# Optimization experiments

Hardware: AMD Instinct MI355X
Metric: run time of the kernel (lower is better)

## Reference

```python
import jax, jax.numpy as jnp
import numpy as np

C = 128        # dim_in = dim_out = dim_mid (exp_ratio=1.0)
HEADS = 4      # C // dim_head
DH = 32        # dim_head
WS = 7         # window_size
EPS = 1e-6
SCALE = DH ** -0.5


def bn3d(x, g, b):
    # BatchNorm3d forward (training-mode batch stats), eps=1e-6
    m = jnp.mean(x, axis=(0, 2, 3, 4), keepdims=True)
    v = jnp.mean((x - m) ** 2, axis=(0, 2, 3, 4), keepdims=True)
    xn = (x - m) * jax.lax.rsqrt(v + EPS)
    return xn * g.reshape(1, -1, 1, 1, 1) + b.reshape(1, -1, 1, 1, 1)


def conv1x1(x, w):
    # 1x1x1 conv, no bias: w is (out, in)
    return jnp.einsum('oi,bihwd->bohwd', w, x)


def setup_inputs() -> dict:
    key = jax.random.key(0)
    ks = jax.random.split(key, 6)
    x = jax.random.normal(ks[0], (4, C, 28, 28, 28), jnp.float32)
    g_in = jnp.ones((C,), jnp.float32)
    b_in = jnp.zeros((C,), jnp.float32)
    w_qk = jax.random.normal(ks[1], (2 * C, C), jnp.float32) * (C ** -0.5)
    w_v = jax.random.normal(ks[2], (C, C), jnp.float32) * (C ** -0.5)
    w_cl = jax.random.normal(ks[3], (C, C, 3, 3, 3), jnp.float32) * ((C * 27) ** -0.5)
    g_cl = jnp.ones((C,), jnp.float32)
    b_cl = jnp.zeros((C,), jnp.float32)
    w_proj = jax.random.normal(ks[4], (C, C), jnp.float32) * (C ** -0.5)
    return {"x": x, "g_in": g_in, "b_in": b_in, "w_qk": w_qk, "w_v": w_v,
            "w_cl": w_cl, "g_cl": g_cl, "b_cl": b_cl, "w_proj": w_proj}


def reference(x, g_in, b_in, w_qk, w_v, w_cl, g_cl, b_cl, w_proj):
    B, Cc, H, W, D = x.shape
    shortcut = x
    x = bn3d(x, g_in, b_in)

    # strided window partition: einops '(h1 n1)' => h1 (window) is the OUTER factor
    n1, n2, n3 = H // WS, W // WS, D // WS  # chosen divisible -> zero pad
    xw = x.reshape(B, Cc, WS, n1, WS, n2, WS, n3)
    xw = xw.transpose(0, 3, 5, 7, 1, 2, 4, 6).reshape(B * n1 * n2 * n3, Cc, WS, WS, WS)
    b = xw.shape[0]
    L = WS ** 3

    # qk: 1x1 conv -> split q,k -> (b, heads, L, dh)
    qk = conv1x1(xw, w_qk).reshape(b, 2, HEADS, DH, L)
    q = qk[:, 0].transpose(0, 1, 3, 2)       # b h L d
    k = qk[:, 1]                             # b h d L
    attn = jax.nn.softmax(jnp.einsum('bhld,bhdm->bhlm', q, k) * SCALE, axis=-1)

    # v: 1x1 conv + relu (attn_pre=False)
    v = jax.nn.relu(conv1x1(xw, w_v)).reshape(b, HEADS, DH, L)  # b h d L
    xs = jnp.einsum('bhlm,bhdm->bhld', attn, v)                 # b h L d
    xs = xs.transpose(0, 1, 3, 2).reshape(b, Cc, WS, WS, WS)

    # reverse window partition
    x = xs.reshape(B, n1, n2, n3, Cc, WS, WS, WS)
    x = x.transpose(0, 4, 5, 1, 6, 2, 7, 3).reshape(B, Cc, H, W, D)

    # local 3x3x3 conv + BN + SiLU, residual (has_skip inside iRMB branch)
    y = jax.lax.conv_general_dilated(
        x, w_cl, window_strides=(1, 1, 1),
        padding=[(1, 1), (1, 1), (1, 1)],
        dimension_numbers=('NCDHW', 'OIDHW', 'NCDHW'))
    y = jax.nn.silu(bn3d(y, g_cl, b_cl))
    x = x + y  # SE is Identity (se_ratio=0)

    x = conv1x1(x, w_proj)
    return shortcut + x
```

## Files before the change

### kernel.cpp

```cpp
#include <hip/hip_runtime.h>
#include <hip/hip_bf16.h>

#define C      128
#define SP     21952
#define PT     87808
#define LW     343
#define EPS_   1e-6f
#define SCALE_ 0.17677669529663687f

#define MISC_A   0
#define MISC_B   128
#define MISC_BQK 256
#define MISC_BV  512
#define MISC_SUM 640
#define MISC_SQ  768
#define MISC_A2  896
#define MISC_B2  1024
#define MISC_XS  1152
#define MISC_XQ  1280

typedef __attribute__((ext_vector_type(8))) short bf16x8;
typedef __attribute__((ext_vector_type(4))) float f32x4;

__device__ __forceinline__ float b2f(unsigned short u){
  return __uint_as_float(((unsigned int)u) << 16);
}
__device__ __forceinline__ unsigned short f2b(float f){
  unsigned int u = __float_as_uint(f);
  u += 0x7fffu + ((u >> 16) & 1u);
  return (unsigned short)(u >> 16);
}

__global__ __launch_bounds__(256) void k0_partial(const float* __restrict__ x,
                                                  float* __restrict__ misc){
  int c = blockIdx.x & 127, chunk = blockIdx.x >> 7;
  int bb = chunk >> 1, half = chunk & 1;
  const float4* p = reinterpret_cast<const float4*>(
      x + (size_t)(bb*C + c)*SP + half*10976);
  int t = threadIdx.x;
  float s = 0.f, ss = 0.f;
  for (int i = t; i < 2744; i += 256){
    float4 v = p[i];
    s  += v.x + v.y + v.z + v.w;
    ss += v.x*v.x + v.y*v.y + v.z*v.z + v.w*v.w;
  }
  #pragma unroll
  for (int off = 32; off > 0; off >>= 1){
    s  += __shfl_xor(s,  off);
    ss += __shfl_xor(ss, off);
  }
  __shared__ float red[8];
  int wid = t >> 6, lane = t & 63;
  if (lane == 0){ red[wid] = s; red[4+wid] = ss; }
  __syncthreads();
  if (t == 0){
    atomicAdd(&misc[MISC_XS + c], red[0]+red[1]+red[2]+red[3]);
    atomicAdd(&misc[MISC_XQ + c], red[4]+red[5]+red[6]+red[7]);
  }
}

__global__ void k1_bias(const float* __restrict__ wqk, const float* __restrict__ wvv,
                        const float* __restrict__ gin, const float* __restrict__ bin,
                        float* __restrict__ misc){
  __shared__ float bv[128];
  int t = threadIdx.x;
  {
    float mean = misc[MISC_XS + t] / (float)PT;
    float var  = misc[MISC_XQ + t] / (float)PT - mean*mean;
    float a = rsqrtf(var + EPS_) * gin[t];
    float bb = bin[t] - mean * a;
    bv[t] = bb;
    if (blockIdx.x == 0){ misc[MISC_A + t] = a; misc[MISC_B + t] = bb; }
  }
  __syncthreads();
  int o = blockIdx.x*128 + t;
  float acc = 0.f;
  if (o < 256){
    const float* wr = wqk + (size_t)o*128;
    for (int c = 0; c < 128; ++c) acc += wr[c]*bv[c];
    misc[MISC_BQK + o] = acc;
  } else {
    const float* wr = wvv + (size_t)(o-256)*128;
    for (int c = 0; c < 128; ++c) acc += wr[c]*bv[c];
    misc[MISC_BV + (o-256)] = acc;
  }
}

__global__ void k1w(const float* __restrict__ wqk, const float* __restrict__ wvv,
                    unsigned short* __restrict__ w2){
  int idx = blockIdx.x*256 + threadIdx.x;
  int o = idx >> 7;
  float w = (o < 256) ? wqk[idx] : wvv[idx - 32768];
  unsigned short h = f2b(w);
  w2[idx] = h;
  w2[49152 + idx] = f2b(w - b2f(h));
}

__global__ __launch_bounds__(256) void k2_qkv(const float* __restrict__ x,
        const unsigned short* __restrict__ w2, const float* __restrict__ misc,
        unsigned short* __restrict__ qg, unsigned short* __restrict__ kg,
        unsigned short* __restrict__ vg){
  __shared__ __align__(16) unsigned short xh[8192];
  __shared__ __align__(16) unsigned short xl[8192];
  __shared__ float ascale[128];
  __shared__ unsigned int posTab[64];
  int t = threadIdx.x;
  int P0 = blockIdx.x * 64;
  int b = P0 / SP, sp0 = P0 % SP;
  if (t < 128) ascale[t] = misc[MISC_A + t];
  if (t < 64){
    int sp = sp0 + t;
    int h_ = sp / 784, rem = sp % 784;
    int w_ = rem / 28, d_ = rem % 28;
    int w1 = h_ & 3, s1 = h_ >> 2;
    int w2i = w_ & 3, s2 = w_ >> 2;
    int w3 = d_ & 3, s3 = d_ >> 2;
    int bw = ((b*4 + w1)*4 + w2i)*4 + w3;
    int l  = (s1*7 + s2)*7 + s3;
    posTab[t] = (unsigned int)(bw*43904 + l*32);
  }
  __syncthreads();
  {
    int p = t & 63;
    int ob = t >> 6;
    const float* xb = x + (size_t)b*C*SP + sp0 + p;
    for (int it = 0; it < 4; ++it){
      int c0 = (ob + it*4) * 8;
      unsigned int ph[4], pl[4];
      #pragma unroll
      for (int j = 0; j < 4; ++j){
        float f0 = xb[(size_t)(c0 + 2*j)*SP]     * ascale[c0 + 2*j];
        float f1 = xb[(size_t)(c0 + 2*j + 1)*SP] * ascale[c0 + 2*j + 1];
        unsigned short h0 = f2b(f0), h1 = f2b(f1);
        unsigned short l0 = f2b(f0 - b2f(h0)), l1 = f2b(f1 - b2f(h1));
        ph[j] = (unsigned int)h0 | ((unsigned int)h1 << 16);
        pl[j] = (unsigned int)l0 | ((unsigned int)l1 << 16);
      }
      int byte = (p*256 + c0*2) ^ ((p & 7) << 4);
      *reinterpret_cast<uint4*>((char*)xh + byte) = make_uint4(ph[0],ph[1],ph[2],ph[3]);
      *reinterpret_cast<uint4*>((char*)xl + byte) = make_uint4(pl[0],pl[1],pl[2],pl[3]);
    }
  }
  __syncthreads();
  int wid = t >> 6, lane = t & 63;
  int g = lane >> 4, ln = lane & 15;
  int wstart = wid * 96;
  f32x4 acc[6][4];
  #pragma unroll
  for (int nt = 0; nt < 6; ++nt){
    float bv = misc[256 + wstart + nt*16 + ln];
    #pragma unroll
    for (int mt = 0; mt < 4; ++mt) acc[nt][mt] = (f32x4){bv,bv,bv,bv};
  }
  #pragma unroll 1
  for (int kk = 0; kk < 4; ++kk){
    bf16x8 ah[4], al[4];
    #pragma unroll
    for (int mt = 0; mt < 4; ++mt){
      int row = mt*16 + ln;
      int byte = (row*256 + kk*64 + g*16) ^ ((ln & 7) << 4);
      ah[mt] = *reinterpret_cast<const bf16x8*>((const char*)xh + byte);
      al[mt] = *reinterpret_cast<const bf16x8*>((const char*)xl + byte);
    }
    #pragma unroll
    for (int nt = 0; nt < 6; ++nt){
      int o = wstart + nt*16 + ln;
      const unsigned short* wp = w2 + (size_t)o*128 + kk*32 + g*8;
      bf16x8 whf = *reinterpret_cast<const bf16x8*>(wp);
      bf16x8 wlf = *reinterpret_cast<const bf16x8*>(wp + 49152);
      #pragma unroll
      for (int mt = 0; mt < 4; ++mt){
        acc[nt][mt] = __builtin_amdgcn_mfma_f32_16x16x32_bf16(ah[mt], whf, acc[nt][mt], 0, 0, 0);
        acc[nt][mt] = __builtin_amdgcn_mfma_f32_16x16x32_bf16(al[mt], whf, acc[nt][mt], 0, 0, 0);
        acc[nt][mt] = __builtin_amdgcn_mfma_f32_16x16x32_bf16(ah[mt], wlf, acc[nt][mt], 0, 0, 0);
      }
    }
  }
  unsigned int ptab[16];
  #pragma unroll
  for (int mt = 0; mt < 4; ++mt)
    #pragma unroll
    for (int r = 0; r < 4; ++r)
      ptab[mt*4+r] = posTab[mt*16 + g*4 + r];
  #pragma unroll
  for (int nt = 0; nt < 6; ++nt){
    int o = wstart + nt*16 + ln;
    bool isv = (o >= 256);
    int oo = o & 127;
    unsigned short* dst = ((o < 128) ? qg : (o < 256 ? kg : vg)) + (oo >> 5)*10976 + (oo & 31);
    #pragma unroll
    for (int mt = 0; mt < 4; ++mt){
      #pragma unroll
      for (int r = 0; r < 4; ++r){
        float v = acc[nt][mt][r];
        if (isv) v = fmaxf(v, 0.f);
        dst[ptab[mt*4+r]] = f2b(v);
      }
    }
  }
}

__global__ __launch_bounds__(256) void k3_attn(const unsigned short* __restrict__ qg,
        const unsigned short* __restrict__ kg, const unsigned short* __restrict__ vg,
        unsigned short* __restrict__ xatt){
  __shared__ __align__(16) unsigned short klds[352*32];
  __shared__ __align__(16) unsigned short vper[32*360];
  __shared__ __align__(16) unsigned short pbuf[4][640];
  int bh = blockIdx.x;
  int bw = bh >> 2, h = bh & 3;
  int t = threadIdx.x;
  int wid = t >> 6, lane = t & 63;
  int g = lane >> 4, ln = lane & 15;
  const unsigned short* kbase = kg + (size_t)bh*LW*32;
  const unsigned short* vbase = vg + (size_t)bh*LW*32;
  const unsigned short* qbase = qg + (size_t)bh*LW*32;
  {
    const uint4* src = reinterpret_cast<const uint4*>(kbase);
    uint4* dst = reinterpret_cast<uint4*>(klds);
    for (int i = t; i < 1372; i += 256) dst[i] = src[i];
    for (int i = t; i < 288; i += 256) klds[10976 + i] = 0;
  }
  for (int idx = t; idx < 10976; idx += 256){
    int m = idx >> 5, d = idx & 31;
    int km = m & 31;
    int pk = ((km & 15) << 1) | (km >> 4);
    vper[d*360 + ((m >> 5) << 5) + pk] = vbase[idx];
  }
  for (int i = t; i < 288; i += 256){
    int m = 343 + (i >> 5), d = i & 31;
    int km = m & 31;
    int pk = ((km & 15) << 1) | (km >> 4);
    vper[d*360 + 320 + pk] = 0;
  }
  __syncthreads();
  int w1 = (bw>>4)&3, w2 = (bw>>2)&3, w3 = bw&3, b = bw>>6;
  unsigned short* pb = pbuf[wid];
  const f32x4 zero4 = {0.f, 0.f, 0.f, 0.f};
  for (int rt = wid; rt < 22; rt += 4){
    int row0 = rt << 4;
    bf16x8 qf = *reinterpret_cast<const bf16x8*>(qbase + (size_t)(row0 + ln)*32 + g*8);
    f32x4 s[22];
    #pragma unroll
    for (int nt = 0; nt < 22; ++nt){
      bf16x8 kf = *reinterpret_cast<const bf16x8*>(&klds[(nt*16 + ln)*32 + g*8]);
      s[nt] = __builtin_amdgcn_mfma_f32_16x16x32_bf16(qf, kf, zero4, 0, 0, 0);
    }
    float mxs[4];
    #pragma unroll
    for (int q = 0; q < 4; ++q){
      float m0 = -1e30f;
      #pragma unroll
      for (int nt = 0; nt < 21; ++nt) m0 = fmaxf(m0, s[nt][q]);
      if (ln < 7) m0 = fmaxf(m0, s[21][q]);
      #pragma unroll
      for (int off = 8; off > 0; off >>= 1) m0 = fmaxf(m0, __shfl_xor(m0, off));
      mxs[q] = m0 * SCALE_;
    }
    f32x4 o0 = zero4, o1 = zero4;
    float sums[4] = {0.f, 0.f, 0.f, 0.f};
    #pragma unroll
    for (int c = 0; c < 11; ++c){
      #pragma unroll
      for (int q = 0; q < 4; ++q){
        float e0 = __expf(fmaf(s[2*c][q],   SCALE_, -mxs[q]));
        float e1 = (c*32 + 16 + ln < 343)
                 ? __expf(fmaf(s[2*c+1][q], SCALE_, -mxs[q])) : 0.f;
        sums[q] += e0 + e1;
        unsigned int pkd;
        asm volatile("v_cvt_pk_bf16_f32 %0, %1, %2" : "=v"(pkd) : "v"(e0), "v"(e1));
        *reinterpret_cast<unsigned int*>(&pb[(g*4+q)*40 + (ln<<1)]) = pkd;
      }
      asm volatile("s_waitcnt lgkmcnt(0)" ::: "memory");
      __builtin_amdgcn_sched_barrier(0);
      bf16x8 pa  = *reinterpret_cast<const bf16x8*>(&pb[ln*40 + g*8]);
      bf16x8 vb0 = *reinterpret_cast<const bf16x8*>(&vper[ln*360       + (c<<5) + g*8]);
      bf16x8 vb1 = *reinterpret_cast<const bf16x8*>(&vper[(16+ln)*360  + (c<<5) + g*8]);
      o0 = __builtin_amdgcn_mfma_f32_16x16x32_bf16(pa, vb0, o0, 0, 0, 0);
      o1 = __builtin_amdgcn_mfma_f32_16x16x32_bf16(pa, vb1, o1, 0, 0, 0);
    }
    float iss[4];
    #pragma unroll
    for (int q = 0; q < 4; ++q){
      float sq = sums[q];
      #pragma unroll
      for (int off = 8; off > 0; off >>= 1) sq += __shfl_xor(sq, off);
      iss[q] = 1.f / sq;
    }
    #pragma unroll
    for (int q = 0; q < 4; ++q){
      int l = row0 + g*4 + q;
      if (l < 343){
        int ss1 = l/49, ss2 = (l/7)%7, ss3 = l%7;
        int sp = (ss1*4+w1)*784 + (ss2*4+w2)*28 + (ss3*4+w3);
        size_t gaddr = ((size_t)b*SP + sp)*128 + h*32;
        xatt[gaddr + ln]      = f2b(o0[q]*iss[q]);
        xatt[gaddr + 16 + ln] = f2b(o1[q]*iss[q]);
      }
    }
  }
}

__global__ void k_wprep(const float* __restrict__ wcl, unsigned short* __restrict__ wbf){
  int f = blockIdx.x*256 + threadIdx.x;
  int j  = f & 7;
  int oc = (f >> 3) & 127;
  int kgr= (f >> 10) & 7;
  int sl = f >> 13;
  int h  = sl / 27, tap = sl % 27;
  int ic = h*64 + kgr*8 + j;
  wbf[f] = f2b(wcl[((size_t)oc*128 + ic)*27 + tap]);
}

__global__ void k6w(const float* __restrict__ wproj, unsigned short* __restrict__ w6){
  int idx = blockIdx.x*256 + threadIdx.x;
  float w = wproj[idx];
  unsigned short h = f2b(w);
  w6[idx] = h;
  w6[16384 + idx] = f2b(w - b2f(h));
}

__global__ __launch_bounds__(128) void k4_mfma(const unsigned short* __restrict__ xag,
        const unsigned short* __restrict__ wbf, unsigned short* __restrict__ yg){
  __shared__ __align__(16) unsigned short halo[8*216*8];
  int t = threadIdx.x, wid = t >> 6, lane = t & 63;
  int g = lane >> 4, ln = lane & 15;
  int stile = blockIdx.x;
  int b = stile / 343, srem = stile % 343;
  int z0 = (srem/49)*4, y0 = ((srem/7)%7)*4, x0 = (srem%7)*4;
  int ohalf = wid;
  int hp = (ln>>2)*6 + (ln&3);
  f32x4 acc[4][4] = {};
  const unsigned short* wb0 = wbf + (size_t)(g*1024 + ohalf*512 + ln*8);
  bf16x8 b0[8], b1[8];

  #define BLOADX(dst_, s_) do { \
    const unsigned short* wp_ = wb0 + (size_t)(s_)*8192; \
    _Pragma("unroll") \
    for (int ks_ = 0; ks_ < 2; ++ks_) \
      _Pragma("unroll") \
      for (int nt_ = 0; nt_ < 4; ++nt_) \
        dst_[ks_*4+nt_] = *reinterpret_cast<const bf16x8*>(wp_ + ks_*4096 + nt_*128); \
  } while(0)

  #define COMPUTE(tap_, buf_) do { \
    int dz_ = (tap_)/9, r9_ = (tap_)%9, dy_ = r9_/3, dx_ = r9_%3; \
    int off_ = dz_*36 + dy_*6 + dx_; \
    bf16x8 af_[2][4]; \
    _Pragma("unroll") \
    for (int ks_ = 0; ks_ < 2; ++ks_) \
      _Pragma("unroll") \
      for (int mt_ = 0; mt_ < 4; ++mt_) \
        af_[ks_][mt_] = *reinterpret_cast<const bf16x8*>( \
            &halo[((ks_*4 + g)*216 + mt_*36 + hp + off_)*8]); \
    _Pragma("unroll") \
    for (int nt_ = 0; nt_ < 4; ++nt_) \
      _Pragma("unroll") \
      for (int ks_ = 0; ks_ < 2; ++ks_) \
        _Pragma("unroll") \
        for (int mt_ = 0; mt_ < 4; ++mt_) \
          acc[nt_][mt_] = __builtin_amdgcn_mfma_f32_16x16x32_bf16( \
              af_[ks_][mt_], buf_[ks_*4+nt_], acc[nt_][mt_], 0, 0, 0); \
  } while(0)

  int s = 0;
  BLOADX(b0, 0);
  for (int h = 0; h < 2; ++h){
    if (h) __syncthreads();
    for (int cidx = t; cidx < 1728; cidx += 128){
      int kgr = cidx / 216, pos = cidx % 216;
      int uz = pos / 36, r36 = pos % 36, uy = r36 / 6, ux = r36 % 6;
      int zz = z0 - 1 + uz, yy = y0 - 1 + uy, xx = x0 - 1 + ux;
      uint4 v = make_uint4(0u,0u,0u,0u);
      if (zz >= 0 && zz < 28 && yy >= 0 && yy < 28 && xx >= 0 && xx < 28)
        v = *reinterpret_cast<const uint4*>(
              &xag[(((size_t)b*SP) + zz*784 + yy*28 + xx)*128 + h*64 + kgr*8]);
      *reinterpret_cast<uint4*>(&halo[(size_t)cidx*8]) = v;
    }
    __syncthreads();
    for (int tp = 0; tp < 26; tp += 2){
      BLOADX(b1, s+1);
      COMPUTE(tp, b0);
      BLOADX(b0, s+2);
      COMPUTE(tp+1, b1);
      s += 2;
    }
    COMPUTE(26, b0);
    ++s;
    if (s < 54) BLOADX(b0, s);
  }
  #pragma unroll
  for (int nt = 0; nt < 4; ++nt){
    int oc = ohalf*64 + nt*16 + ln;
    #pragma unroll
    for (int mt = 0; mt < 4; ++mt){
      #pragma unroll
      for (int r = 0; r < 4; ++r){
        int pos = (z0 + mt)*784 + (y0 + g)*28 + (x0 + r);
        yg[((size_t)b*SP + pos)*128 + oc] = f2b(acc[nt][mt][r]);
      }
    }
  }
  #undef BLOADX
  #undef COMPUTE
}

__global__ __launch_bounds__(256) void k5_ystats(const unsigned short* __restrict__ yg,
                                                 float* __restrict__ misc){
  int t = threadIdx.x;
  int c8 = t & 15;
  int pr = t >> 4;
  float s[8] = {0,0,0,0,0,0,0,0}, q[8] = {0,0,0,0,0,0,0,0};
  size_t base = (size_t)blockIdx.x * 256;
  for (int i = 0; i < 16; ++i){
    size_t pos = base + i*16 + pr;
    uint4 v = *reinterpret_cast<const uint4*>(yg + pos*128 + c8*8);
    #pragma unroll
    for (int j = 0; j < 4; ++j){
      unsigned int u = (&v.x)[j];
      float f0 = __uint_as_float(u << 16);
      float f1 = __uint_as_float(u & 0xffff0000u);
      s[2*j]   += f0; q[2*j]   += f0*f0;
      s[2*j+1] += f1; q[2*j+1] += f1*f1;
    }
  }
  #pragma unroll
  for (int j = 0; j < 8; ++j){
    s[j] += __shfl_xor(s[j], 16); q[j] += __shfl_xor(q[j], 16);
    s[j] += __shfl_xor(s[j], 32); q[j] += __shfl_xor(q[j], 32);
  }
  __shared__ float rs[128], rq[128];
  if (t < 128){ rs[t] = 0.f; rq[t] = 0.f; }
  __syncthreads();
  if ((t & 48) == 0){
    #pragma unroll
    for (int j = 0; j < 8; ++j){
      atomicAdd(&rs[c8*8+j], s[j]);
      atomicAdd(&rq[c8*8+j], q[j]);
    }
  }
  __syncthreads();
  if (t < 128){
    atomicAdd(&misc[MISC_SUM + t], rs[t]);
    atomicAdd(&misc[MISC_SQ  + t], rq[t]);
  }
}

__global__ void k5b_finstats(const float* __restrict__ gcl, const float* __restrict__ bcl,
                             float* __restrict__ misc){
  int c = threadIdx.x;
  float mean = misc[MISC_SUM+c] / (float)PT;
  float var  = misc[MISC_SQ +c] / (float)PT - mean*mean;
  float a = gcl[c] * rsqrtf(var + EPS_);
  misc[MISC_A2+c] = a;
  misc[MISC_B2+c] = bcl[c] - mean*a;
}

__global__ __launch_bounds__(256) void k6_final(const unsigned short* __restrict__ xag,
        const unsigned short* __restrict__ yg, const unsigned short* __restrict__ w6,
        const float* __restrict__ xin, const float* __restrict__ misc,
        float* __restrict__ out){
  __shared__ __align__(16) unsigned short xh[8192];
  __shared__ __align__(16) unsigned short xl[8192];
  __shared__ float a2s[128], b2s[128];
  int t = threadIdx.x;
  int P0 = blockIdx.x * 64;
  int b = P0 / SP, sp0 = P0 % SP;
  if (t < 128){ a2s[t] = misc[MISC_A2+t]; b2s[t] = misc[MISC_B2+t]; }
  __syncthreads();
  for (int idx = t; idx < 1024; idx += 256){
    int p = idx >> 4, c0 = (idx & 15) * 8;
    size_t gb = (size_t)(P0 + p)*128 + c0;
    uint4 yv4 = *reinterpret_cast<const uint4*>(yg + gb);
    uint4 xa4 = *reinterpret_cast<const uint4*>(xag + gb);
    unsigned int ph[4], pl[4];
    #pragma unroll
    for (int j = 0; j < 4; ++j){
      unsigned int uy = (&yv4.x)[j], ux = (&xa4.x)[j];
      int c = c0 + 2*j;
      float y0 = __uint_as_float(uy << 16)          * a2s[c]   + b2s[c];
      float y1 = __uint_as_float(uy & 0xffff0000u)  * a2s[c+1] + b2s[c+1];
      float v0 = __uint_as_float(ux << 16)         + y0 / (1.f + __expf(-y0));
      float v1 = __uint_as_float(ux & 0xffff0000u) + y1 / (1.f + __expf(-y1));
      unsigned short h0 = f2b(v0), h1 = f2b(v1);
      unsigned short l0 = f2b(v0 - b2f(h0)), l1 = f2b(v1 - b2f(h1));
      ph[j] = (unsigned int)h0 | ((unsigned int)h1 << 16);
      pl[j] = (unsigned int)l0 | ((unsigned int)l1 << 16);
    }
    int byte = (p*256 + c0*2) ^ ((p & 7) << 4);
    *reinterpret_cast<uint4*>((char*)xh + byte) = make_uint4(ph[0],ph[1],ph[2],ph[3]);
    *reinterpret_cast<uint4*>((char*)xl + byte) = make_uint4(pl[0],pl[1],pl[2],pl[3]);
  }
  __syncthreads();
  int wid = t >> 6, lane = t & 63;
  int g = lane >> 4, ln = lane & 15;
  f32x4 acc[2][4] = {};
  #pragma unroll 1
  for (int kk = 0; kk < 4; ++kk){
    bf16x8 bh[4], bl[4];
    #pragma unroll
    for (int pt = 0; pt < 4; ++pt){
      int row = pt*16 + ln;
      int byte = (row*256 + kk*64 + g*16) ^ ((ln & 7) << 4);
      bh[pt] = *reinterpret_cast<const bf16x8*>((const char*)xh + byte);
      bl[pt] = *reinterpret_cast<const bf16x8*>((const char*)xl + byte);
    }
    #pragma unroll
    for (int ot = 0; ot < 2; ++ot){
      int o = wid*32 + ot*16 + ln;
      const unsigned short* wp = w6 + (size_t)o*128 + kk*32 + g*8;
      bf16x8 wh = *reinterpret_cast<const bf16x8*>(wp);
      bf16x8 wl = *reinterpret_cast<const bf16x8*>(wp + 16384);
      #pragma unroll
      for (int pt = 0; pt < 4; ++pt){
        acc[ot][pt] = __builtin_amdgcn_mfma_f32_16x16x32_bf16(wh, bh[pt], acc[ot][pt], 0, 0, 0);
        acc[ot][pt] = __builtin_amdgcn_mfma_f32_16x16x32_bf16(wl, bh[pt], acc[ot][pt], 0, 0, 0);
        acc[ot][pt] = __builtin_amdgcn_mfma_f32_16x16x32_bf16(wh, bl[pt], acc[ot][pt], 0, 0, 0);
      }
    }
  }
  #pragma unroll
  for (int ot = 0; ot < 2; ++ot){
    #pragma unroll
    for (int r = 0; r < 4; ++r){
      int o = wid*32 + ot*16 + g*4 + r;
      size_t gbase = ((size_t)b*128 + o)*SP + sp0;
      #pragma unroll
      for (int pt = 0; pt < 4; ++pt){
        size_t gaddr = gbase + pt*16 + ln;
        out[gaddr] = xin[gaddr] + acc[ot][pt][r];
      }
    }
  }
}

extern "C" void kernel_launch(void* const* d_in, const int* in_sizes, int n_in,
                              void* d_out, int out_size, void* d_ws, size_t ws_size,
                              hipStream_t stream){
  const float* x      = (const float*)d_in[0];
  const float* g_in   = (const float*)d_in[1];
  const float* b_in   = (const float*)d_in[2];
  const float* w_qk   = (const float*)d_in[3];
  const float* w_v    = (const float*)d_in[4];
  const float* w_cl   = (const float*)d_in[5];
  const float* g_cl   = (const float*)d_in[6];
  const float* b_cl   = (const float*)d_in[7];
  const float* w_proj = (const float*)d_in[8];
  float* out = (float*)d_out;

  char* ws = (char*)d_ws;
  unsigned short* qg  = (unsigned short*)ws;
  unsigned short* kgp = qg  + 11239424;
  unsigned short* vg  = kgp + 11239424;
  unsigned short* xag = vg  + 11239424;
  unsigned short* yg  = xag + 11239424;
  float* misc = (float*)(ws + (size_t)5*22478848);
  unsigned short* wbf = qg;
  unsigned short* w6  = qg + 524288;
  unsigned short* w2  = yg;

  hipMemsetAsync(misc + MISC_SUM, 0, 768*sizeof(float), stream);
  k0_partial  <<<1024, 256, 0, stream>>>(x, misc);
  k1_bias     <<<3, 128, 0, stream>>>(w_qk, w_v, g_in, b_in, misc);
  k1w         <<<192, 256, 0, stream>>>(w_qk, w_v, w2);
  k2_qkv      <<<1372, 256, 0, stream>>>(x, w2, misc, qg, kgp, vg);
  k3_attn     <<<1024, 256, 0, stream>>>(qg, kgp, vg, xag);
  k_wprep     <<<1728, 256, 0, stream>>>(w_cl, wbf);
  k6w         <<<64, 256, 0, stream>>>(w_proj, w6);
  k4_mfma     <<<1372, 128, 0, stream>>>(xag, wbf, yg);
  k5_ystats   <<<343, 256, 0, stream>>>(yg, misc);
  k5b_finstats<<<1, 128, 0, stream>>>(g_cl, b_cl, misc);
  k6_final    <<<1372, 256, 0, stream>>>(xag, yg, w6, x, misc, out);
}
```

Baseline: 391.7 us.

## Split conv3d MFMA K across waves with LDS reduction and persistent grid

The 3x3x3 conv MFMA kernel now runs 256 threads per block. Each pair of waves splits the 64-channel K chunk, and their partial accumulators are summed through shared memory before the output is written. The grid becomes persistent: 768 blocks loop over 1372 spatial tiles. Scheduling group barriers interleave the LDS reads, global loads and MFMAs. The aim is to halve per-wave register pressure and the weight loads so occupancy and latency hiding improve. In exchange it adds an LDS reduction, extra barriers, and an uneven tile distribution across blocks.

After: 363.5 us. 1.08x faster.

```diff
diff --git a/kernel.cpp b/kernel.cpp
--- a/kernel.cpp
+++ b/kernel.cpp
@@ -319,89 +319,116 @@
   w6[16384 + idx] = f2b(w - b2f(h));
 }
 
-__global__ __launch_bounds__(128) void k4_mfma(const unsigned short* __restrict__ xag,
+__global__ __launch_bounds__(256, 3) void k4_mfma(const unsigned short* __restrict__ xag,
         const unsigned short* __restrict__ wbf, unsigned short* __restrict__ yg){
-  __shared__ __align__(16) unsigned short halo[8*216*8];
+  __shared__ __align__(16) unsigned char smem[32768];
+  unsigned short* halo = (unsigned short*)smem;
+  float* redf = (float*)smem;
   int t = threadIdx.x, wid = t >> 6, lane = t & 63;
   int g = lane >> 4, ln = lane & 15;
-  int stile = blockIdx.x;
-  int b = stile / 343, srem = stile % 343;
-  int z0 = (srem/49)*4, y0 = ((srem/7)%7)*4, x0 = (srem%7)*4;
-  int ohalf = wid;
+  int ks = wid & 1, ohalf = wid >> 1;
   int hp = (ln>>2)*6 + (ln&3);
-  f32x4 acc[4][4] = {};
-  const unsigned short* wb0 = wbf + (size_t)(g*1024 + ohalf*512 + ln*8);
-  bf16x8 b0[8], b1[8];
+  const unsigned short* wb0 = wbf + (size_t)(ks*4096 + g*1024 + ohalf*512 + ln*8);
+  bf16x8 b0[4], b1[4];
+  f32x4 acc[4][4];
 
   #define BLOADX(dst_, s_) do { \
     const unsigned short* wp_ = wb0 + (size_t)(s_)*8192; \
     _Pragma("unroll") \
-    for (int ks_ = 0; ks_ < 2; ++ks_) \
-      _Pragma("unroll") \
-      for (int nt_ = 0; nt_ < 4; ++nt_) \
-        dst_[ks_*4+nt_] = *reinterpret_cast<const bf16x8*>(wp_ + ks_*4096 + nt_*128); \
+    for (int nt_ = 0; nt_ < 4; ++nt_) \
+      dst_[nt_] = *reinterpret_cast<const bf16x8*>(wp_ + nt_*128); \
   } while(0)
 
   #define COMPUTE(tap_, buf_) do { \
     int dz_ = (tap_)/9, r9_ = (tap_)%9, dy_ = r9_/3, dx_ = r9_%3; \
     int off_ = dz_*36 + dy_*6 + dx_; \
-    bf16x8 af_[2][4]; \
+    bf16x8 af_[4]; \
     _Pragma("unroll") \
-    for (int ks_ = 0; ks_ < 2; ++ks_) \
-      _Pragma("unroll") \
-      for (int mt_ = 0; mt_ < 4; ++mt_) \
-        af_[ks_][mt_] = *reinterpret_cast<const bf16x8*>( \
-            &halo[((ks_*4 + g)*216 + mt_*36 + hp + off_)*8]); \
+    for (int mt_ = 0; mt_ < 4; ++mt_) \
+      af_[mt_] = *reinterpret_cast<const bf16x8*>( \
+          &halo[((ks*4 + g)*216 + mt_*36 + hp + off_)*8]); \
     _Pragma("unroll") \
     for (int nt_ = 0; nt_ < 4; ++nt_) \
       _Pragma("unroll") \
-      for (int ks_ = 0; ks_ < 2; ++ks_) \
-        _Pragma("unroll") \
-        for (int mt_ = 0; mt_ < 4; ++mt_) \
-          acc[nt_][mt_] = __builtin_amdgcn_mfma_f32_16x16x32_bf16( \
-              af_[ks_][mt_], buf_[ks_*4+nt_], acc[nt_][mt_], 0, 0, 0); \
+      for (int mt_ = 0; mt_ < 4; ++mt_) \
+        acc[nt_][mt_] = __builtin_amdgcn_mfma_f32_16x16x32_bf16( \
+            af_[mt_], buf_[nt_], acc[nt_][mt_], 0, 0, 0); \
   } while(0)
 
-  int s = 0;
+  #define SGB_TAP() do { \
+    __builtin_amdgcn_sched_group_barrier(0x020, 4, 0);    \
+    __builtin_amdgcn_sched_group_barrier(0x100, 4, 0);    \
+    __builtin_amdgcn_sched_group_barrier(0x008, 16, 0);   \
+  } while(0)
+
   BLOADX(b0, 0);
-  for (int h = 0; h < 2; ++h){
-    if (h) __syncthreads();
-    for (int cidx = t; cidx < 1728; cidx += 128){
-      int kgr = cidx / 216, pos = cidx % 216;
-      int uz = pos / 36, r36 = pos % 36, uy = r36 / 6, ux = r36 % 6;
-      int zz = z0 - 1 + uz, yy = y0 - 1 + uy, xx = x0 - 1 + ux;
-      uint4 v = make_uint4(0u,0u,0u,0u);
-      if (zz >= 0 && zz < 28 && yy >= 0 && yy < 28 && xx >= 0 && xx < 28)
-        v = *reinterpret_cast<const uint4*>(
-              &xag[(((size_t)b*SP) + zz*784 + yy*28 + xx)*128 + h*64 + kgr*8]);
-      *reinterpret_cast<uint4*>(&halo[(size_t)cidx*8]) = v;
+  for (int s = blockIdx.x; s < 1372; s += 768){
+    int b = s / 343, srem = s % 343;
+    int z0 = (srem/49)*4, y0 = ((srem/7)%7)*4, x0 = (srem%7)*4;
+    #pragma unroll
+    for (int nt = 0; nt < 4; ++nt)
+      #pragma unroll
+      for (int mt = 0; mt < 4; ++mt)
+        acc[nt][mt] = (f32x4){0.f, 0.f, 0.f, 0.f};
+    for (int h = 0; h < 2; ++h){
+      __syncthreads();
+      for (int ci = t; ci < 1728; ci += 256){
+        int kgr = ci / 216, pos = ci % 216;
+        int uz = pos / 36, r36 = pos % 36, uy = r36 / 6, ux = r36 % 6;
+        int zz = z0 - 1 + uz, yy = y0 - 1 + uy, xx = x0 - 1 + ux;
+        uint4 v = make_uint4(0u,0u,0u,0u);
+        if (zz >= 0 && zz < 28 && yy >= 0 && yy < 28 && xx >= 0 && xx < 28)
+          v = *reinterpret_cast<const uint4*>(
+                &xag[(((size_t)b*SP) + zz*784 + yy*28 + xx)*128 + h*64 + kgr*8]);
+        *reinterpret_cast<uint4*>(&halo[(size_t)ci*8]) = v;
+      }
+      __syncthreads();
+      int sw = h*27;
+      for (int tp = 0; tp < 26; tp += 2){
+        BLOADX(b1, sw+tp+1);
+        COMPUTE(tp, b0);
+        SGB_TAP();
+        BLOADX(b0, sw+tp+2);
+        COMPUTE(tp+1, b1);
+        SGB_TAP();
+      }
+      BLOADX(b1, (sw + 27) % 54);
+      COMPUTE(26, b0);
+      SGB_TAP();
+      #pragma unroll
+      for (int j = 0; j < 4; ++j) b0[j] = b1[j];
     }
     __syncthreads();
-    for (int tp = 0; tp < 26; tp += 2){
-      BLOADX(b1, s+1);
-      COMPUTE(tp, b0);
-      BLOADX(b0, s+2);
-      COMPUTE(tp+1, b1);
-      s += 2;
-    }
-    COMPUTE(26, b0);
-    ++s;
-    if (s < 54) BLOADX(b0, s);
-  }
-  #pragma unroll
-  for (int nt = 0; nt < 4; ++nt){
-    int oc = ohalf*64 + nt*16 + ln;
-    #pragma unroll
-    for (int mt = 0; mt < 4; ++mt){
-      #pragma unroll
-      for (int r = 0; r < 4; ++r){
-        int pos = (z0 + mt)*784 + (y0 + g)*28 + (x0 + r);
-        yg[((size_t)b*SP + pos)*128 + oc] = f2b(acc[nt][mt][r]);
+    if (ks == 1){
+      #pragma unroll
+      for (int nt = 0; nt < 4; ++nt)
+        #pragma unroll
+        for (int mt = 0; mt < 4; ++mt)
+          *reinterpret_cast<f32x4*>(
+              &redf[(((ohalf*16 + nt*4 + mt)*64) + lane)*4]) = acc[nt][mt];
+    }
+    __syncthreads();
+    if (ks == 0){
+      #pragma unroll
+      for (int nt = 0; nt < 4; ++nt){
+        int oc = ohalf*64 + nt*16 + ln;
+        #pragma unroll
+        for (int mt = 0; mt < 4; ++mt){
+          f32x4 other = *reinterpret_cast<const f32x4*>(
+              &redf[(((ohalf*16 + nt*4 + mt)*64) + lane)*4]);
+          f32x4 tot = acc[nt][mt] + other;
+          #pragma unroll
+          for (int r = 0; r < 4; ++r){
+            int pos = (z0 + mt)*784 + (y0 + g)*28 + (x0 + r);
+            yg[((size_t)b*SP + pos)*128 + oc] = f2b(tot[r]);
+          }
+        }
       }
     }
   }
   #undef BLOADX
   #undef COMPUTE
+  #undef SGB_TAP
 }
 
 __global__ __launch_bounds__(256) void k5_ystats(const unsigned short* __restrict__ yg,
@@ -566,7 +593,7 @@
   k3_attn     <<<1024, 256, 0, stream>>>(qg, kgp, vg, xag);
   k_wprep     <<<1728, 256, 0, stream>>>(w_cl, wbf);
   k6w         <<<64, 256, 0, stream>>>(w_proj, w6);
-  k4_mfma     <<<1372, 128, 0, stream>>>(xag, wbf, yg);
+  k4_mfma     <<<768, 256, 0, stream>>>(xag, wbf, yg);
   k5_ystats   <<<343, 256, 0, stream>>>(yg, misc);
   k5b_finstats<<<1, 128, 0, stream>>>(g_cl, b_cl, misc);
   k6_final    <<<1372, 256, 0, stream>>>(xag, yg, w6, x, misc, out);
```
